# Optimization experiments

Measured on AMD Instinct MI355X. Metric: run time of the kernel, lower is better.

## Reference

```python
import jax, jax.numpy as jnp
import numpy as np

B, S, H, F_IN = 256, 128, 512, 1


def _lstm_step(h, c, x, Wih, Whh, b):
    # PyTorch LSTM gate order: i, f, g, o
    gates = x @ Wih.T + h @ Whh.T + b  # (B, 4H)
    i, f, g, o = jnp.split(gates, 4, axis=-1)
    c = jax.nn.sigmoid(f) * c + jax.nn.sigmoid(i) * jnp.tanh(g)
    h = jax.nn.sigmoid(o) * jnp.tanh(c)
    return h, c


def setup_inputs() -> dict:
    key = jax.random.key(0)
    ks = jax.random.split(key, 18)
    p = lambda k, shape: (jax.random.normal(k, shape, dtype=jnp.float32) * 0.05)
    return {
        "input_seq": jax.random.normal(ks[0], (B, S, F_IN), dtype=jnp.float32),
        # encoder: embedding Linear(F_IN -> H) + LSTM(H -> H)
        "We_e": p(ks[1], (H, F_IN)), "be_e": p(ks[2], (H,)),
        "Wih_e": p(ks[3], (4 * H, H)), "Whh_e": p(ks[4], (4 * H, H)), "b_e": p(ks[5], (4 * H,)),
        # decoder: embedding Linear(F_IN -> H) + LSTMCell(H -> H)
        "We_d": p(ks[6], (H, F_IN)), "be_d": p(ks[7], (H,)),
        "Wih_d": p(ks[8], (4 * H, H)), "Whh_d": p(ks[9], (4 * H, H)), "b_d": p(ks[10], (4 * H,)),
        # additive attention: W_1, W_2 (H->H), v (H->1)
        "W1": p(ks[11], (H, H)), "b1": p(ks[12], (H,)),
        "W2": p(ks[13], (H, H)), "b2": p(ks[14], (H,)),
        "v": p(ks[15], (1, H)), "bv": p(ks[16], (1,)),
    }


def reference(input_seq, We_e, be_e, Wih_e, Whh_e, b_e,
              We_d, be_d, Wih_d, Whh_d, b_d,
              W1, b1, W2, b2, v, bv):
    # ---- encoder: embed then LSTM over the sequence ----
    emb = input_seq @ We_e.T + be_e  # (B, S, H)

    def enc_step(carry, x_t):
        h, c = carry
        h, c = _lstm_step(h, c, x_t, Wih_e, Whh_e, b_e)
        return (h, c), h

    h0 = jnp.zeros((B, H), dtype=input_seq.dtype)
    (h, c), enc_h = jax.lax.scan(enc_step, (h0, h0), jnp.swapaxes(emb, 0, 1))
    encoder_output = jnp.swapaxes(enc_h, 0, 1)  # (B, S, H)

    # W_1(encoder_output) is loop-invariant; hoist it (same math as the
    # original, which redundantly recomputes it every step).
    w1enc = encoder_output @ W1.T + b1  # (B, S, H)

    # ---- decoder: per-step LSTMCell + additive attention ----
    def dec_step(carry, _):
        hd, cd, x_in = carry
        e = x_in @ We_d.T + be_d  # (B, H)
        hd, cd = _lstm_step(hd, cd, e, Wih_d, Whh_d, b_d)
        q = hd @ W2.T + b2  # (B, H)
        u = jnp.squeeze(jnp.tanh(w1enc + q[:, None, :]) @ v.T + bv, -1)  # (B, S)
        att = jax.nn.log_softmax(u, axis=1)
        idx = jnp.argmax(att, axis=1)  # pointer (B,)
        # next decoder input = pointed-to input symbol
        x_next = jnp.take_along_axis(input_seq[:, :, 0], idx[:, None], axis=1)  # (B, 1)
        return (hd, cd, x_next), (att, idx)

    x0 = jnp.zeros((B, 1), dtype=input_seq.dtype)
    _, (scores, ptrs) = jax.lax.scan(dec_step, (h, c, x0), None, length=S)
    pointers_scores = jnp.swapaxes(scores, 0, 1)  # (B, S, S) log-probs
    pointers = jnp.swapaxes(ptrs, 0, 1)  # (B, S) int
    return pointers_scores, pointers
```

## Files before the change

### kernel.cpp

```cpp
#include <hip/hip_runtime.h>
#include <hip/hip_bf16.h>
#include <hip/hip_fp16.h>

#define Bn 256
#define Sn 128
#define Hn 512
#define G4 2048
#define BT 16
#define HT 16

__device__ __forceinline__ float sigf(float x){
    float e = expf(-fabsf(x));
    float d = 1.f + e;
    return x >= 0.f ? 1.f/d : e/d;
}

__global__ void precompute_kernel(
    const float* __restrict__ Wih_e, const float* __restrict__ We_e,
    const float* __restrict__ be_e,  const float* __restrict__ b_e,
    const float* __restrict__ Wih_d, const float* __restrict__ We_d,
    const float* __restrict__ be_d,  const float* __restrict__ b_d,
    float* __restrict__ p1, float* __restrict__ p0,
    float* __restrict__ r1, float* __restrict__ r0)
{
    int j = blockIdx.x*blockDim.x + threadIdx.x;
    bool dec = j >= G4;
    int jj = dec ? j - G4 : j;
    const float* Wih = dec ? Wih_d : Wih_e;
    const float* We  = dec ? We_d  : We_e;
    const float* be  = dec ? be_d  : be_e;
    const float* bb  = dec ? b_d   : b_e;
    float s1 = 0.f, s0 = 0.f;
    for (int k = 0; k < Hn; ++k) {
        float w = Wih[jj*Hn + k];
        s1 += w * We[k];
        s0 += w * be[k];
    }
    s0 += bb[jj];
    if (dec) { r1[jj] = s1; r0[jj] = s0; }
    else     { p1[jj] = s1; p0[jj] = s0; }
}

template<int MODE, bool WE_F32>
__global__ __launch_bounds__(256) void lstm_step_kernel(
    const float* __restrict__ h_prev,
    float* __restrict__ h_next,
    float* __restrict__ cbuf,
    const float* __restrict__ Whh,
    const float* __restrict__ P1,
    const float* __restrict__ P0,
    const float* __restrict__ xseq,
    const float* __restrict__ x_in,
    const float* __restrict__ W1,
    const float* __restrict__ b1,
    void* __restrict__ w1enc,
    int t)
{
    __shared__ float hs[Hn][BT+1];
    const int tid = threadIdx.x;
    const int b0 = blockIdx.x * BT;
    const int h0 = blockIdx.y * HT;
    const int lane_b = tid & (BT-1);
    const int hth = tid >> 4;

    for (int idx = tid; idx < BT*Hn; idx += 256) {
        int bb2 = idx >> 9;
        int k  = idx & (Hn-1);
        hs[k][bb2] = h_prev[(b0+bb2)*Hn + k];
    }
    __syncthreads();

    const int hg = h0 + hth;
    constexpr int NACC = (MODE==0) ? 5 : 4;
    float acc[NACC];
    #pragma unroll
    for (int g = 0; g < NACC; ++g) acc[g] = 0.f;
    const float* wrow[NACC];
    #pragma unroll
    for (int g = 0; g < 4; ++g) wrow[g] = Whh + (size_t)(g*Hn + hg)*Hn;
    if constexpr (MODE == 0) wrow[4] = W1 + (size_t)hg*Hn;

    for (int k = 0; k < Hn; k += 8) {
        float hv[8];
        #pragma unroll
        for (int j = 0; j < 8; ++j) hv[j] = hs[k+j][lane_b];
        #pragma unroll
        for (int g = 0; g < NACC; ++g) {
            float4 wa = *(const float4*)(wrow[g] + k);
            float4 wb = *(const float4*)(wrow[g] + k + 4);
            acc[g] += hv[0]*wa.x + hv[1]*wa.y + hv[2]*wa.z + hv[3]*wa.w
                    + hv[4]*wb.x + hv[5]*wb.y + hv[6]*wb.z + hv[7]*wb.w;
        }
    }

    const int b_glob = b0 + lane_b;
    float xv = (MODE==0) ? xseq[b_glob*Sn + t] : x_in[b_glob];
    float gi = acc[0] + xv*P1[0*Hn+hg] + P0[0*Hn+hg];
    float gf = acc[1] + xv*P1[1*Hn+hg] + P0[1*Hn+hg];
    float gg = acc[2] + xv*P1[2*Hn+hg] + P0[2*Hn+hg];
    float go = acc[3] + xv*P1[3*Hn+hg] + P0[3*Hn+hg];
    size_t off = (size_t)b_glob*Hn + hg;
    float cold = cbuf[off];
    float cn = sigf(gf)*cold + sigf(gi)*tanhf(gg);
    float hn = sigf(go)*tanhf(cn);
    cbuf[off] = cn;
    h_next[off] = hn;
    if constexpr (MODE == 0) {
        if (t > 0) {
            size_t widx = (size_t)b_glob*(Sn*Hn) + (size_t)(t-1)*Hn + hg;
            float val = acc[4] + b1[hg];
            if constexpr (WE_F32) ((float*)w1enc)[widx] = val;
            else                  ((__half*)w1enc)[widx] = __float2half(val);
        }
    }
}

template<bool OF32>
__global__ __launch_bounds__(256) void linear_kernel(
    const float* __restrict__ hin,
    const float* __restrict__ W,
    const float* __restrict__ bias,
    void* __restrict__ outp,
    int ostride, int ooff)
{
    __shared__ float hs[Hn][BT+1];
    const int tid = threadIdx.x;
    const int b0 = blockIdx.x * BT;
    const int n0 = blockIdx.y * HT;
    const int lane_b = tid & (BT-1);
    const int hth = tid >> 4;
    for (int idx = tid; idx < BT*Hn; idx += 256) {
        int bb2 = idx >> 9;
        int k  = idx & (Hn-1);
        hs[k][bb2] = hin[(b0+bb2)*Hn + k];
    }
    __syncthreads();
    const int ng = n0 + hth;
    const float* wr = W + (size_t)ng*Hn;
    float acc = 0.f;
    for (int k = 0; k < Hn; k += 8) {
        float4 wa = *(const float4*)(wr + k);
        float4 wb = *(const float4*)(wr + k + 4);
        acc += hs[k+0][lane_b]*wa.x + hs[k+1][lane_b]*wa.y
             + hs[k+2][lane_b]*wa.z + hs[k+3][lane_b]*wa.w
             + hs[k+4][lane_b]*wb.x + hs[k+5][lane_b]*wb.y
             + hs[k+6][lane_b]*wb.z + hs[k+7][lane_b]*wb.w;
    }
    float val = acc + bias[ng];
    size_t oidx = (size_t)(b0+lane_b)*ostride + ooff + ng;
    if constexpr (OF32) ((float*)outp)[oidx] = val;
    else                ((__half*)outp)[oidx] = __float2half(val);
}

template<bool WE_F32>
__global__ __launch_bounds__(512) void attn_kernel(
    const void* __restrict__ w1enc,
    const float* __restrict__ q,
    const float* __restrict__ v,
    const float* __restrict__ xseq,
    float* __restrict__ out_scores,
    float* __restrict__ out_ptr,
    float* __restrict__ x_in,
    int t)
{
    __shared__ float qs[Hn], vs[Hn], us[Sn], red[2];
    const int b = blockIdx.x;
    const int tid = threadIdx.x;
    if (tid < Hn) { qs[tid] = q[b*Hn + tid]; vs[tid] = v[tid]; }
    __syncthreads();
    const int wave = tid >> 6, l = tid & 63;
    const int sub = l >> 5, kl = l & 31;
    const int k0 = kl*16;
    for (int si = 0; si < 8; ++si) {
        int s = si*16 + wave*2 + sub;
        float w[16];
        if constexpr (WE_F32) {
            const float* wr = (const float*)w1enc + ((size_t)b*Sn + s)*Hn + k0;
            #pragma unroll
            for (int i = 0; i < 16; i += 4) {
                float4 wv = *(const float4*)(wr + i);
                w[i+0]=wv.x; w[i+1]=wv.y; w[i+2]=wv.z; w[i+3]=wv.w;
            }
        } else {
            const __half* wr = (const __half*)w1enc + ((size_t)b*Sn + s)*Hn + k0;
            #pragma unroll
            for (int i = 0; i < 16; i += 8) {
                uint4 u = *(const uint4*)(wr + i);
                float2 f0 = __half22float2(*(const __half2*)&u.x);
                float2 f1 = __half22float2(*(const __half2*)&u.y);
                float2 f2 = __half22float2(*(const __half2*)&u.z);
                float2 f3 = __half22float2(*(const __half2*)&u.w);
                w[i+0]=f0.x; w[i+1]=f0.y; w[i+2]=f1.x; w[i+3]=f1.y;
                w[i+4]=f2.x; w[i+5]=f2.y; w[i+6]=f3.x; w[i+7]=f3.y;
            }
        }
        float a = 0.f;
        #pragma unroll
        for (int i = 0; i < 16; ++i)
            a += vs[k0+i]*tanhf(w[i] + qs[k0+i]);
        #pragma unroll
        for (int off2 = 1; off2 <= 16; off2 <<= 1) a += __shfl_xor(a, off2);
        if (kl == 0) us[s] = a;
    }
    __syncthreads();
    if (wave == 0) {
        float a = us[l], c2 = us[l+64];
        float mv; int mi;
        if (c2 > a) { mv = c2; mi = l+64; } else { mv = a; mi = l; }
        #pragma unroll
        for (int off2 = 1; off2 < 64; off2 <<= 1) {
            float ov = __shfl_xor(mv, off2);
            int   oi = __shfl_xor(mi, off2);
            if (ov > mv || (ov == mv && oi < mi)) { mv = ov; mi = oi; }
        }
        float es = expf(a - mv) + expf(c2 - mv);
        #pragma unroll
        for (int off2 = 1; off2 < 64; off2 <<= 1) es += __shfl_xor(es, off2);
        if (l == 0) {
            red[0] = mv; red[1] = logf(es);
            out_ptr[b*Sn + t] = (float)mi;
            x_in[b] = xseq[b*Sn + mi];
        }
    }
    __syncthreads();
    if (tid < Sn) {
        out_scores[(size_t)b*Sn*Sn + (size_t)t*Sn + tid] =
            us[tid] - red[0] - red[1];
    }
}

extern "C" void kernel_launch(void* const* d_in, const int* in_sizes, int n_in,
                              void* d_out, int out_size, void* d_ws, size_t ws_size,
                              hipStream_t stream)
{
    const float* input_seq = (const float*)d_in[0];
    const float* We_e = (const float*)d_in[1],  *be_e = (const float*)d_in[2];
    const float* Wih_e = (const float*)d_in[3], *Whh_e = (const float*)d_in[4];
    const float* b_e = (const float*)d_in[5];
    const float* We_d = (const float*)d_in[6],  *be_d = (const float*)d_in[7];
    const float* Wih_d = (const float*)d_in[8], *Whh_d = (const float*)d_in[9];
    const float* b_d = (const float*)d_in[10];
    const float* W1 = (const float*)d_in[11], *b1 = (const float*)d_in[12];
    const float* W2 = (const float*)d_in[13], *b2 = (const float*)d_in[14];
    const float* v  = (const float*)d_in[15];

    float* ws = (float*)d_ws;
    size_t o = 0;
    float* hb0  = ws + o; o += Bn*Hn;
    float* hb1  = ws + o; o += Bn*Hn;
    float* cbuf = ws + o; o += Bn*Hn;
    float* qbuf = ws + o; o += Bn*Hn;
    float* p1   = ws + o; o += G4;
    float* p0   = ws + o; o += G4;
    float* r1   = ws + o; o += G4;
    float* r0   = ws + o; o += G4;
    float* x_in = ws + o; o += 256;
    void* w1enc = (void*)(ws + o);
    const size_t w1enc_elems = (size_t)Bn*Sn*Hn;
    const size_t need_f32 = (o + w1enc_elems) * sizeof(float);
    const bool wf32 = (ws_size >= need_f32);

    hipMemsetAsync(hb0,  0, Bn*Hn*sizeof(float), stream);
    hipMemsetAsync(cbuf, 0, Bn*Hn*sizeof(float), stream);
    hipMemsetAsync(x_in, 0, Bn*sizeof(float), stream);

    precompute_kernel<<<dim3(16), 256, 0, stream>>>(Wih_e, We_e, be_e, b_e,
                                                    Wih_d, We_d, be_d, b_d,
                                                    p1, p0, r1, r0);

    dim3 gtile(Bn/BT, Hn/HT);
    float* hprev = hb0; float* hnext = hb1;
    for (int t = 0; t < Sn; ++t) {
        if (wf32)
            lstm_step_kernel<0,true ><<<gtile, 256, 0, stream>>>(hprev, hnext, cbuf, Whh_e,
                                                                 p1, p0, input_seq, nullptr,
                                                                 W1, b1, w1enc, t);
        else
            lstm_step_kernel<0,false><<<gtile, 256, 0, stream>>>(hprev, hnext, cbuf, Whh_e,
                                                                 p1, p0, input_seq, nullptr,
                                                                 W1, b1, w1enc, t);
        float* tmp = hprev; hprev = hnext; hnext = tmp;
    }
    if (wf32)
        linear_kernel<true ><<<gtile, 256, 0, stream>>>(hprev, W1, b1, w1enc,
                                                        Sn*Hn, (Sn-1)*Hn);
    else
        linear_kernel<false><<<gtile, 256, 0, stream>>>(hprev, W1, b1, w1enc,
                                                        Sn*Hn, (Sn-1)*Hn);

    float* out_scores = (float*)d_out;
    float* out_ptr = out_scores + (size_t)Bn*Sn*Sn;

    for (int t = 0; t < Sn; ++t) {
        if (wf32) {
            lstm_step_kernel<1,true ><<<gtile, 256, 0, stream>>>(hprev, hnext, cbuf, Whh_d,
                                                                 r1, r0, nullptr, x_in,
                                                                 nullptr, nullptr, nullptr, t);
            linear_kernel<true ><<<gtile, 256, 0, stream>>>(hnext, W2, b2, qbuf, Hn, 0);
            attn_kernel<true ><<<dim3(Bn), 512, 0, stream>>>(w1enc, qbuf, v, input_seq,
                                                             out_scores, out_ptr, x_in, t);
        } else {
            lstm_step_kernel<1,false><<<gtile, 256, 0, stream>>>(hprev, hnext, cbuf, Whh_d,
                                                                 r1, r0, nullptr, x_in,
                                                                 nullptr, nullptr, nullptr, t);
            linear_kernel<true ><<<gtile, 256, 0, stream>>>(hnext, W2, b2, qbuf, Hn, 0);
            attn_kernel<false><<<dim3(Bn), 512, 0, stream>>>(w1enc, qbuf, v, input_seq,
                                                             out_scores, out_ptr, x_in, t);
        }
        float* tmp = hprev; hprev = hnext; hnext = tmp;
    }
}
```

Measured before the change: 13.95 ms.

## Fuse encoder/decoder steps into one persistent kernel with grid barriers

```diff
diff --git a/kernel.cpp b/kernel.cpp
--- a/kernel.cpp
+++ b/kernel.cpp
@@ -1,18 +1,30 @@
 #include <hip/hip_runtime.h>
-#include <hip/hip_bf16.h>
 #include <hip/hip_fp16.h>
 
 #define Bn 256
 #define Sn 128
 #define Hn 512
 #define G4 2048
-#define BT 16
-#define HT 16
+#define NBLK 256
+#define NTHR 1024
+#define HSTR 516
 
 __device__ __forceinline__ float sigf(float x){
     float e = expf(-fabsf(x));
     float d = 1.f + e;
     return x >= 0.f ? 1.f/d : e/d;
+}
+
+__device__ __forceinline__ void gbar(unsigned int* cnt, unsigned int target){
+    __syncthreads();
+    if (threadIdx.x == 0) {
+        __threadfence();
+        __hip_atomic_fetch_add(cnt, 1u, __ATOMIC_RELEASE, __HIP_MEMORY_SCOPE_AGENT);
+        while (__hip_atomic_load(cnt, __ATOMIC_ACQUIRE, __HIP_MEMORY_SCOPE_AGENT) < target)
+            __builtin_amdgcn_s_sleep(4);
+        __threadfence();
+    }
+    __syncthreads();
 }
 
 __global__ void precompute_kernel(
@@ -41,192 +53,215 @@
     else     { p1[jj] = s1; p0[jj] = s0; }
 }
 
-template<int MODE, bool WE_F32>
-__global__ __launch_bounds__(256) void lstm_step_kernel(
-    const float* __restrict__ h_prev,
-    float* __restrict__ h_next,
-    float* __restrict__ cbuf,
-    const float* __restrict__ Whh,
-    const float* __restrict__ P1,
-    const float* __restrict__ P0,
+template<bool WEF>
+__global__ __launch_bounds__(NTHR, 4) void ptrnet_kernel(
     const float* __restrict__ xseq,
-    const float* __restrict__ x_in,
-    const float* __restrict__ W1,
-    const float* __restrict__ b1,
-    void* __restrict__ w1enc,
-    int t)
+    const float* __restrict__ Whh_e, const float* __restrict__ Whh_d,
+    const float* __restrict__ W1, const float* __restrict__ b1,
+    const float* __restrict__ W2, const float* __restrict__ b2,
+    const float* __restrict__ vv,
+    const float* __restrict__ p1, const float* __restrict__ p0,
+    const float* __restrict__ r1, const float* __restrict__ r0,
+    float* __restrict__ hb0, float* __restrict__ hb1,
+    float* __restrict__ cbuf, float* __restrict__ qbuf,
+    float* __restrict__ x_in, void* __restrict__ w1enc,
+    unsigned int* __restrict__ barcnt,
+    float* __restrict__ out_scores, float* __restrict__ out_ptr)
 {
-    __shared__ float hs[Hn][BT+1];
+    __shared__ float smem[16*HSTR + 512*5 + 16];
+    float* hs  = smem;
+    float* red = smem + 16*HSTR;
+    float* qs  = smem;
+    float* vs  = smem + Hn;
+    float* us  = smem + 2*Hn;
+    float* rr  = smem + 2*Hn + Sn + 8;
+
+    const int blk = blockIdx.x;
     const int tid = threadIdx.x;
-    const int b0 = blockIdx.x * BT;
-    const int h0 = blockIdx.y * HT;
-    const int lane_b = tid & (BT-1);
-    const int hth = tid >> 4;
-
-    for (int idx = tid; idx < BT*Hn; idx += 256) {
-        int bb2 = idx >> 9;
-        int k  = idx & (Hn-1);
-        hs[k][bb2] = h_prev[(b0+bb2)*Hn + k];
+    const int bt  = blk >> 4, grp = blk & 15;
+    const int b0  = bt << 4;
+    const int tb  = tid & 15;
+    const int hh  = (tid >> 4) & 31;
+    const int ks  = tid >> 9;
+    const int hg  = (grp << 5) + hh;
+    const int kofs = ks << 8;
+    unsigned int tgt = 0;
+    float* hprev = hb0;
+    float* hnext = hb1;
+
+#define STAGE_H(SRC) do { \
+    for (int i_ = tid; i_ < 16*128; i_ += NTHR) { \
+        int row_ = i_ >> 7; int c4_ = (i_ & 127) << 2; \
+        *(float4*)(hs + row_*HSTR + c4_) = \
+            *(const float4*)((SRC) + (size_t)(b0+row_)*Hn + c4_); \
+    } __syncthreads(); } while(0)
+
+    for (int t = 0; t <= Sn; ++t) {
+        STAGE_H(hprev);
+        float a0=0.f,a1=0.f,a2=0.f,a3=0.f,a4=0.f;
+        {
+            const float* hrow = hs + tb*HSTR + kofs;
+            const float* w0 = Whh_e + (size_t)hg*Hn          + kofs;
+            const float* w1r= Whh_e + (size_t)(Hn+hg)*Hn     + kofs;
+            const float* w2r= Whh_e + (size_t)(2*Hn+hg)*Hn   + kofs;
+            const float* w3r= Whh_e + (size_t)(3*Hn+hg)*Hn   + kofs;
+            const float* w4r= W1    + (size_t)hg*Hn          + kofs;
+            for (int i = 0; i < 256; i += 4) {
+                float4 hv = *(const float4*)(hrow + i);
+                float4 x0 = *(const float4*)(w0 + i);
+                float4 x1 = *(const float4*)(w1r + i);
+                float4 x2 = *(const float4*)(w2r + i);
+                float4 x3 = *(const float4*)(w3r + i);
+                float4 x4 = *(const float4*)(w4r + i);
+                a0 += hv.x*x0.x + hv.y*x0.y + hv.z*x0.z + hv.w*x0.w;
+                a1 += hv.x*x1.x + hv.y*x1.y + hv.z*x1.z + hv.w*x1.w;
+                a2 += hv.x*x2.x + hv.y*x2.y + hv.z*x2.z + hv.w*x2.w;
+                a3 += hv.x*x3.x + hv.y*x3.y + hv.z*x3.z + hv.w*x3.w;
+                a4 += hv.x*x4.x + hv.y*x4.y + hv.z*x4.z + hv.w*x4.w;
+            }
+        }
+        if (ks) {
+            float* rp = red + (size_t)(tid - 512)*5;
+            rp[0]=a0; rp[1]=a1; rp[2]=a2; rp[3]=a3; rp[4]=a4;
+        }
+        __syncthreads();
+        if (!ks) {
+            const float* rp = red + (size_t)tid*5;
+            a0+=rp[0]; a1+=rp[1]; a2+=rp[2]; a3+=rp[3]; a4+=rp[4];
+            size_t off = (size_t)(b0+tb)*Hn + hg;
+            if (t < Sn) {
+                float xv = xseq[(b0+tb)*Sn + t];
+                float gi = a0 + xv*p1[hg]      + p0[hg];
+                float gf = a1 + xv*p1[Hn+hg]   + p0[Hn+hg];
+                float gg = a2 + xv*p1[2*Hn+hg] + p0[2*Hn+hg];
+                float go = a3 + xv*p1[3*Hn+hg] + p0[3*Hn+hg];
+                float cn = sigf(gf)*cbuf[off] + sigf(gi)*tanhf(gg);
+                float hn = sigf(go)*tanhf(cn);
+                cbuf[off] = cn; hnext[off] = hn;
+            }
+            if (t > 0) {
+                size_t widx = ((size_t)(b0+tb)*Sn + (t-1))*Hn + hg;
+                float val = a4 + b1[hg];
+                if constexpr (WEF) ((float*)w1enc)[widx] = val;
+                else               ((__half*)w1enc)[widx] = __float2half(val);
+            }
+        }
+        tgt += NBLK; gbar(barcnt, tgt);
+        if (t < Sn) { float* tp = hprev; hprev = hnext; hnext = tp; }
     }
-    __syncthreads();
-
-    const int hg = h0 + hth;
-    constexpr int NACC = (MODE==0) ? 5 : 4;
-    float acc[NACC];
-    #pragma unroll
-    for (int g = 0; g < NACC; ++g) acc[g] = 0.f;
-    const float* wrow[NACC];
-    #pragma unroll
-    for (int g = 0; g < 4; ++g) wrow[g] = Whh + (size_t)(g*Hn + hg)*Hn;
-    if constexpr (MODE == 0) wrow[4] = W1 + (size_t)hg*Hn;
-
-    for (int k = 0; k < Hn; k += 8) {
-        float hv[8];
-        #pragma unroll
-        for (int j = 0; j < 8; ++j) hv[j] = hs[k+j][lane_b];
-        #pragma unroll
-        for (int g = 0; g < NACC; ++g) {
-            float4 wa = *(const float4*)(wrow[g] + k);
-            float4 wb = *(const float4*)(wrow[g] + k + 4);
-            acc[g] += hv[0]*wa.x + hv[1]*wa.y + hv[2]*wa.z + hv[3]*wa.w
-                    + hv[4]*wb.x + hv[5]*wb.y + hv[6]*wb.z + hv[7]*wb.w;
-        }
-    }
-
-    const int b_glob = b0 + lane_b;
-    float xv = (MODE==0) ? xseq[b_glob*Sn + t] : x_in[b_glob];
-    float gi = acc[0] + xv*P1[0*Hn+hg] + P0[0*Hn+hg];
-    float gf = acc[1] + xv*P1[1*Hn+hg] + P0[1*Hn+hg];
-    float gg = acc[2] + xv*P1[2*Hn+hg] + P0[2*Hn+hg];
-    float go = acc[3] + xv*P1[3*Hn+hg] + P0[3*Hn+hg];
-    size_t off = (size_t)b_glob*Hn + hg;
-    float cold = cbuf[off];
-    float cn = sigf(gf)*cold + sigf(gi)*tanhf(gg);
-    float hn = sigf(go)*tanhf(cn);
-    cbuf[off] = cn;
-    h_next[off] = hn;
-    if constexpr (MODE == 0) {
-        if (t > 0) {
-            size_t widx = (size_t)b_glob*(Sn*Hn) + (size_t)(t-1)*Hn + hg;
-            float val = acc[4] + b1[hg];
-            if constexpr (WE_F32) ((float*)w1enc)[widx] = val;
-            else                  ((__half*)w1enc)[widx] = __float2half(val);
-        }
-    }
-}
-
-template<bool OF32>
-__global__ __launch_bounds__(256) void linear_kernel(
-    const float* __restrict__ hin,
-    const float* __restrict__ W,
-    const float* __restrict__ bias,
-    void* __restrict__ outp,
-    int ostride, int ooff)
-{
-    __shared__ float hs[Hn][BT+1];
-    const int tid = threadIdx.x;
-    const int b0 = blockIdx.x * BT;
-    const int n0 = blockIdx.y * HT;
-    const int lane_b = tid & (BT-1);
-    const int hth = tid >> 4;
-    for (int idx = tid; idx < BT*Hn; idx += 256) {
-        int bb2 = idx >> 9;
-        int k  = idx & (Hn-1);
-        hs[k][bb2] = hin[(b0+bb2)*Hn + k];
-    }
-    __syncthreads();
-    const int ng = n0 + hth;
-    const float* wr = W + (size_t)ng*Hn;
-    float acc = 0.f;
-    for (int k = 0; k < Hn; k += 8) {
-        float4 wa = *(const float4*)(wr + k);
-        float4 wb = *(const float4*)(wr + k + 4);
-        acc += hs[k+0][lane_b]*wa.x + hs[k+1][lane_b]*wa.y
-             + hs[k+2][lane_b]*wa.z + hs[k+3][lane_b]*wa.w
-             + hs[k+4][lane_b]*wb.x + hs[k+5][lane_b]*wb.y
-             + hs[k+6][lane_b]*wb.z + hs[k+7][lane_b]*wb.w;
-    }
-    float val = acc + bias[ng];
-    size_t oidx = (size_t)(b0+lane_b)*ostride + ooff + ng;
-    if constexpr (OF32) ((float*)outp)[oidx] = val;
-    else                ((__half*)outp)[oidx] = __float2half(val);
-}
-
-template<bool WE_F32>
-__global__ __launch_bounds__(512) void attn_kernel(
-    const void* __restrict__ w1enc,
-    const float* __restrict__ q,
-    const float* __restrict__ v,
-    const float* __restrict__ xseq,
-    float* __restrict__ out_scores,
-    float* __restrict__ out_ptr,
-    float* __restrict__ x_in,
-    int t)
-{
-    __shared__ float qs[Hn], vs[Hn], us[Sn], red[2];
-    const int b = blockIdx.x;
-    const int tid = threadIdx.x;
-    if (tid < Hn) { qs[tid] = q[b*Hn + tid]; vs[tid] = v[tid]; }
-    __syncthreads();
-    const int wave = tid >> 6, l = tid & 63;
-    const int sub = l >> 5, kl = l & 31;
-    const int k0 = kl*16;
-    for (int si = 0; si < 8; ++si) {
-        int s = si*16 + wave*2 + sub;
-        float w[16];
-        if constexpr (WE_F32) {
-            const float* wr = (const float*)w1enc + ((size_t)b*Sn + s)*Hn + k0;
-            #pragma unroll
-            for (int i = 0; i < 16; i += 4) {
-                float4 wv = *(const float4*)(wr + i);
-                w[i+0]=wv.x; w[i+1]=wv.y; w[i+2]=wv.z; w[i+3]=wv.w;
+
+    for (int t = 0; t < Sn; ++t) {
+        STAGE_H(hprev);
+        float a0=0.f,a1=0.f,a2=0.f,a3=0.f;
+        {
+            const float* hrow = hs + tb*HSTR + kofs;
+            const float* w0 = Whh_d + (size_t)hg*Hn        + kofs;
+            const float* w1r= Whh_d + (size_t)(Hn+hg)*Hn   + kofs;
+            const float* w2r= Whh_d + (size_t)(2*Hn+hg)*Hn + kofs;
+            const float* w3r= Whh_d + (size_t)(3*Hn+hg)*Hn + kofs;
+            for (int i = 0; i < 256; i += 4) {
+                float4 hv = *(const float4*)(hrow + i);
+                float4 x0 = *(const float4*)(w0 + i);
+                float4 x1 = *(const float4*)(w1r + i);
+                float4 x2 = *(const float4*)(w2r + i);
+                float4 x3 = *(const float4*)(w3r + i);
+                a0 += hv.x*x0.x + hv.y*x0.y + hv.z*x0.z + hv.w*x0.w;
+                a1 += hv.x*x1.x + hv.y*x1.y + hv.z*x1.z + hv.w*x1.w;
+                a2 += hv.x*x2.x + hv.y*x2.y + hv.z*x2.z + hv.w*x2.w;
+                a3 += hv.x*x3.x + hv.y*x3.y + hv.z*x3.z + hv.w*x3.w;
+            }
+        }
+        if (ks) {
+            float* rp = red + (size_t)(tid - 512)*4;
+            rp[0]=a0; rp[1]=a1; rp[2]=a2; rp[3]=a3;
+        }
+        __syncthreads();
+        if (!ks) {
+            const float* rp = red + (size_t)tid*4;
+            a0+=rp[0]; a1+=rp[1]; a2+=rp[2]; a3+=rp[3];
+            size_t off = (size_t)(b0+tb)*Hn + hg;
+            float xv = x_in[b0+tb];
+            float gi = a0 + xv*r1[hg]      + r0[hg];
+            float gf = a1 + xv*r1[Hn+hg]   + r0[Hn+hg];
+            float gg = a2 + xv*r1[2*Hn+hg] + r0[2*Hn+hg];
+            float go = a3 + xv*r1[3*Hn+hg] + r0[3*Hn+hg];
+            float cn = sigf(gf)*cbuf[off] + sigf(gi)*tanhf(gg);
+            float hn = sigf(go)*tanhf(cn);
+            cbuf[off] = cn; hnext[off] = hn;
+        }
+        tgt += NBLK; gbar(barcnt, tgt);
+        { float* tp = hprev; hprev = hnext; hnext = tp; }
+
+        STAGE_H(hprev);
+        float qa = 0.f;
+        {
+            const float* hrow = hs + tb*HSTR + kofs;
+            const float* wq = W2 + (size_t)hg*Hn + kofs;
+            for (int i = 0; i < 256; i += 4) {
+                float4 hv = *(const float4*)(hrow + i);
+                float4 wv = *(const float4*)(wq + i);
+                qa += hv.x*wv.x + hv.y*wv.y + hv.z*wv.z + hv.w*wv.w;
+            }
+        }
+        if (ks) red[tid - 512] = qa;
+        __syncthreads();
+        if (!ks) qbuf[(size_t)(b0+tb)*Hn + hg] = qa + red[tid] + b2[hg];
+        tgt += NBLK; gbar(barcnt, tgt);
+
+        if (tid < Hn) qs[tid] = qbuf[(size_t)blk*Hn + tid];
+        else          vs[tid - Hn] = vv[tid - Hn];
+        __syncthreads();
+        const int s = tid >> 3, ksl = tid & 7, kb = ksl << 6;
+        float a = 0.f;
+        if constexpr (WEF) {
+            const float* wr = (const float*)w1enc + ((size_t)blk*Sn + s)*Hn + kb;
+            for (int i = 0; i < 64; i += 4) {
+                float4 w4 = *(const float4*)(wr + i);
+                a += vs[kb+i+0]*tanhf(w4.x + qs[kb+i+0]);
+                a += vs[kb+i+1]*tanhf(w4.y + qs[kb+i+1]);
+                a += vs[kb+i+2]*tanhf(w4.z + qs[kb+i+2]);
+                a += vs[kb+i+3]*tanhf(w4.w + qs[kb+i+3]);
             }
         } else {
-            const __half* wr = (const __half*)w1enc + ((size_t)b*Sn + s)*Hn + k0;
-            #pragma unroll
-            for (int i = 0; i < 16; i += 8) {
-                uint4 u = *(const uint4*)(wr + i);
+            const __half* wr = (const __half*)w1enc + ((size_t)blk*Sn + s)*Hn + kb;
+            for (int i = 0; i < 64; i += 4) {
+                uint2 u = *(const uint2*)(wr + i);
                 float2 f0 = __half22float2(*(const __half2*)&u.x);
                 float2 f1 = __half22float2(*(const __half2*)&u.y);
-                float2 f2 = __half22float2(*(const __half2*)&u.z);
-                float2 f3 = __half22float2(*(const __half2*)&u.w);
-                w[i+0]=f0.x; w[i+1]=f0.y; w[i+2]=f1.x; w[i+3]=f1.y;
-                w[i+4]=f2.x; w[i+5]=f2.y; w[i+6]=f3.x; w[i+7]=f3.y;
-            }
-        }
-        float a = 0.f;
-        #pragma unroll
-        for (int i = 0; i < 16; ++i)
-            a += vs[k0+i]*tanhf(w[i] + qs[k0+i]);
-        #pragma unroll
-        for (int off2 = 1; off2 <= 16; off2 <<= 1) a += __shfl_xor(a, off2);
-        if (kl == 0) us[s] = a;
+                a += vs[kb+i+0]*tanhf(f0.x + qs[kb+i+0]);
+                a += vs[kb+i+1]*tanhf(f0.y + qs[kb+i+1]);
+                a += vs[kb+i+2]*tanhf(f1.x + qs[kb+i+2]);
+                a += vs[kb+i+3]*tanhf(f1.y + qs[kb+i+3]);
+            }
+        }
+        a += __shfl_xor(a, 1); a += __shfl_xor(a, 2); a += __shfl_xor(a, 4);
+        if (ksl == 0) us[s] = a;
+        __syncthreads();
+        if (tid < 64) {
+            float av = us[tid], c2 = us[tid+64];
+            float mv; int mi;
+            if (c2 > av) { mv = c2; mi = tid+64; } else { mv = av; mi = tid; }
+            #pragma unroll
+            for (int off2 = 1; off2 < 64; off2 <<= 1) {
+                float ov = __shfl_xor(mv, off2);
+                int   oi = __shfl_xor(mi, off2);
+                if (ov > mv || (ov == mv && oi < mi)) { mv = ov; mi = oi; }
+            }
+            float es = expf(av - mv) + expf(c2 - mv);
+            #pragma unroll
+            for (int off2 = 1; off2 < 64; off2 <<= 1) es += __shfl_xor(es, off2);
+            if (tid == 0) {
+                rr[0] = mv; rr[1] = logf(es);
+                out_ptr[blk*Sn + t] = (float)mi;
+                x_in[blk] = xseq[blk*Sn + mi];
+            }
+        }
+        __syncthreads();
+        if (tid < Sn)
+            out_scores[((size_t)blk*Sn + t)*Sn + tid] = us[tid] - rr[0] - rr[1];
+        if (t < Sn-1) { tgt += NBLK; gbar(barcnt, tgt); }
     }
-    __syncthreads();
-    if (wave == 0) {
-        float a = us[l], c2 = us[l+64];
-        float mv; int mi;
-        if (c2 > a) { mv = c2; mi = l+64; } else { mv = a; mi = l; }
-        #pragma unroll
-        for (int off2 = 1; off2 < 64; off2 <<= 1) {
-            float ov = __shfl_xor(mv, off2);
-            int   oi = __shfl_xor(mi, off2);
-            if (ov > mv || (ov == mv && oi < mi)) { mv = ov; mi = oi; }
-        }
-        float es = expf(a - mv) + expf(c2 - mv);
-        #pragma unroll
-        for (int off2 = 1; off2 < 64; off2 <<= 1) es += __shfl_xor(es, off2);
-        if (l == 0) {
-            red[0] = mv; red[1] = logf(es);
-            out_ptr[b*Sn + t] = (float)mi;
-            x_in[b] = xseq[b*Sn + mi];
-        }
-    }
-    __syncthreads();
-    if (tid < Sn) {
-        out_scores[(size_t)b*Sn*Sn + (size_t)t*Sn + tid] =
-            us[tid] - red[0] - red[1];
-    }
+#undef STAGE_H
 }
 
 extern "C" void kernel_launch(void* const* d_in, const int* in_sizes, int n_in,
@@ -255,6 +290,7 @@
     float* r1   = ws + o; o += G4;
     float* r0   = ws + o; o += G4;
     float* x_in = ws + o; o += 256;
+    unsigned int* barcnt = (unsigned int*)(ws + o); o += 64;
     void* w1enc = (void*)(ws + o);
     const size_t w1enc_elems = (size_t)Bn*Sn*Hn;
     const size_t need_f32 = (o + w1enc_elems) * sizeof(float);
@@ -262,51 +298,20 @@
 
     hipMemsetAsync(hb0,  0, Bn*Hn*sizeof(float), stream);
     hipMemsetAsync(cbuf, 0, Bn*Hn*sizeof(float), stream);
-    hipMemsetAsync(x_in, 0, Bn*sizeof(float), stream);
+    hipMemsetAsync(x_in, 0, (256+64)*sizeof(float), stream);
 
     precompute_kernel<<<dim3(16), 256, 0, stream>>>(Wih_e, We_e, be_e, b_e,
                                                     Wih_d, We_d, be_d, b_d,
                                                     p1, p0, r1, r0);
 
-    dim3 gtile(Bn/BT, Hn/HT);
-    float* hprev = hb0; float* hnext = hb1;
-    for (int t = 0; t < Sn; ++t) {
-        if (wf32)
-            lstm_step_kernel<0,true ><<<gtile, 256, 0, stream>>>(hprev, hnext, cbuf, Whh_e,
-                                                                 p1, p0, input_seq, nullptr,
-                                                                 W1, b1, w1enc, t);
-        else
-            lstm_step_kernel<0,false><<<gtile, 256, 0, stream>>>(hprev, hnext, cbuf, Whh_e,
-                                                                 p1, p0, input_seq, nullptr,
-                                                                 W1, b1, w1enc, t);
-        float* tmp = hprev; hprev = hnext; hnext = tmp;
-    }
     if (wf32)
-        linear_kernel<true ><<<gtile, 256, 0, stream>>>(hprev, W1, b1, w1enc,
-                                                        Sn*Hn, (Sn-1)*Hn);
+        ptrnet_kernel<true ><<<dim3(NBLK), dim3(NTHR), 0, stream>>>(
+            input_seq, Whh_e, Whh_d, W1, b1, W2, b2, v,
+            p1, p0, r1, r0, hb0, hb1, cbuf, qbuf, x_in, w1enc, barcnt,
+            (float*)d_out, (float*)d_out + (size_t)Bn*Sn*Sn);
     else
-        linear_kernel<false><<<gtile, 256, 0, stream>>>(hprev, W1, b1, w1enc,
-                                                        Sn*Hn, (Sn-1)*Hn);
-
-    float* out_scores = (float*)d_out;
-    float* out_ptr = out_scores + (size_t)Bn*Sn*Sn;
-
-    for (int t = 0; t < Sn; ++t) {
-        if (wf32) {
-            lstm_step_kernel<1,true ><<<gtile, 256, 0, stream>>>(hprev, hnext, cbuf, Whh_d,
-                                                                 r1, r0, nullptr, x_in,
-                                                                 nullptr, nullptr, nullptr, t);
-            linear_kernel<true ><<<gtile, 256, 0, stream>>>(hnext, W2, b2, qbuf, Hn, 0);
-            attn_kernel<true ><<<dim3(Bn), 512, 0, stream>>>(w1enc, qbuf, v, input_seq,
-                                                             out_scores, out_ptr, x_in, t);
-        } else {
-            lstm_step_kernel<1,false><<<gtile, 256, 0, stream>>>(hprev, hnext, cbuf, Whh_d,
-                                                                 r1, r0, nullptr, x_in,
-                                                                 nullptr, nullptr, nullptr, t);
-            linear_kernel<true ><<<gtile, 256, 0, stream>>>(hnext, W2, b2, qbuf, Hn, 0);
-            attn_kernel<false><<<dim3(Bn), 512, 0, stream>>>(w1enc, qbuf, v, input_seq,
-                                                             out_scores, out_ptr, x_in, t);
-        }
-        float* tmp = hprev; hprev = hnext; hnext = tmp;
-    }
-}
+        ptrnet_kernel<false><<<dim3(NBLK), dim3(NTHR), 0, stream>>>(
+            input_seq, Whh_e, Whh_d, W1, b1, W2, b2, v,
+            p1, p0, r1, r0, hb0, hb1, cbuf, qbuf, x_in, w1enc, barcnt,
+            (float*)d_out, (float*)d_out + (size_t)Bn*Sn*Sn);
+}
```

Result: slower. 50.37 ms (+261.0%).
